# Optimization experiments

Measured on AMD Instinct MI355X. Metric: run time of the kernel, lower is better.

Reference implementation:

```python
import jax, jax.numpy as jnp
import numpy as np

AVG_STEP_WEIGHTING = 0.002


def _mean_rbf_kernel(a, b):
    """Mean over all (i,j) of exp(-||a_i - b_j||^2 / 2), features flattened.

    Equivalent to the original per-row loop: (1/N) * sum_i mean_j k(b, a_i).
    Uses the Gram trick to avoid materializing (N, M, D) intermediates.
    """
    A = a.reshape(a.shape[0], -1)  # (N, D)
    B = b.reshape(b.shape[0], -1)  # (M, D)
    sq_a = jnp.sum(A * A, axis=1)  # (N,)
    sq_b = jnp.sum(B * B, axis=1)  # (M,)
    # (N, M) pairwise squared distances; clamp tiny negatives from fp error
    d2 = jnp.maximum(sq_a[:, None] + sq_b[None, :] - 2.0 * (A @ B.T), 0.0)
    return jnp.mean(jnp.exp(-0.5 * d2))


def setup_inputs() -> dict:
    key = jax.random.key(0)
    kx, ky = jax.random.split(key)
    N, M, D1, D2 = 4096, 4096, 24, 8
    x = jax.random.normal(kx, (N, D1, D2), dtype=jnp.float32)
    y = jax.random.normal(ky, (M, D1, D2), dtype=jnp.float32)
    avg_step = jnp.asarray(5.0, dtype=jnp.float32)
    return {"x": x, "y": y, "avg_step": avg_step}


def reference(x, y, avg_step):
    XX = _mean_rbf_kernel(x, x)
    XY = _mean_rbf_kernel(x, y)
    YY = _mean_rbf_kernel(y, y)
    mmd = XX + YY - 2.0 * XY
    loss = mmd + (jnp.maximum(jnp.asarray(1.0, x.dtype), avg_step) - 1.0) * AVG_STEP_WEIGHTING
    return (loss, mmd)
```

## Files before the change

### kernel.cpp

```cpp
#include <hip/hip_runtime.h>
#include <hip/hip_bf16.h>

typedef __attribute__((ext_vector_type(8))) short short8;
typedef __attribute__((ext_vector_type(4))) float float4v;

#define N_ROWS 4096
#define K_DIM  192
#define TILE   128
#define NT     32
#define NSYM   528
#define NBLK   2080
#define LDSS   104
#define C1     (-0.72134752044448179f)
#define LOG2E  (1.4426950408889634f)

__global__ void prep_kernel(const float* __restrict__ x, const float* __restrict__ y,
                            __hip_bfloat16* __restrict__ xb, __hip_bfloat16* __restrict__ yb,
                            float* __restrict__ sqx, float* __restrict__ sqy)
{
    int w    = (blockIdx.x * blockDim.x + threadIdx.x) >> 6;
    int lane = threadIdx.x & 63;
    if (w >= 2 * N_ROWS) return;
    const float*      src = (w < N_ROWS) ? (x + (size_t)w * K_DIM) : (y + (size_t)(w - N_ROWS) * K_DIM);
    __hip_bfloat16*   dst = (w < N_ROWS) ? (xb + (size_t)w * K_DIM) : (yb + (size_t)(w - N_ROWS) * K_DIM);
    float s = 0.f;
    #pragma unroll
    for (int i = 0; i < 3; ++i) {
        float f = src[lane + 64 * i];
        __hip_bfloat16 h = __float2bfloat16(f);
        dst[lane + 64 * i] = h;
        float fb = __bfloat162float(h);
        s += fb * fb;
    }
    #pragma unroll
    for (int off = 32; off; off >>= 1) s += __shfl_down(s, off, 64);
    if (lane == 0) {
        if (w < N_ROWS) sqx[w] = s; else sqy[w - N_ROWS] = s;
    }
}

__global__ void gram_kernel(const __hip_bfloat16* __restrict__ xb, const __hip_bfloat16* __restrict__ yb,
                            const float* __restrict__ sqx, const float* __restrict__ sqy,
                            float* __restrict__ partials)
{
    __shared__ short lA[TILE * LDSS];
    __shared__ short lB[TILE * LDSS];
    __shared__ float wred[4];

    const short* xbs = (const short*)xb;
    const short* ybs = (const short*)yb;

    int id = blockIdx.x;
    const short *A, *B; const float *sa, *sb;
    int bi, bj;
    float weight = 1.0f;
    if (id < 2 * NSYM) {
        int t;
        if (id < NSYM) { t = id;        A = xbs; B = xbs; sa = sqx; sb = sqx; }
        else           { t = id - NSYM; A = ybs; B = ybs; sa = sqy; sb = sqy; }
        bi = 0;
        while (t >= NT - bi) { t -= NT - bi; ++bi; }
        bj = bi + t;
        if (bi != bj) weight = 2.0f;
    } else {
        int t = id - 2 * NSYM;
        bi = t >> 5; bj = t & 31;
        A = xbs; B = ybs; sa = sqx; sb = sqy;
    }
    const int abase = bi * TILE, bbase = bj * TILE;

    const int tid  = threadIdx.x;
    const int lane = tid & 63, w = tid >> 6;
    const int wm   = w >> 1,  wn = w & 1;
    const int m15  = lane & 15, quad = lane >> 4;

    float4v acc[4][4];
    #pragma unroll
    for (int i = 0; i < 4; ++i)
        #pragma unroll
        for (int j = 0; j < 4; ++j) acc[i][j] = (float4v){0.f, 0.f, 0.f, 0.f};

    for (int s = 0; s < 2; ++s) {
        const int k0 = s * 96;
        if (s) __syncthreads();
        #pragma unroll
        for (int it = 0; it < 6; ++it) {
            int c   = it * 256 + tid;
            int row = c / 12;
            int cw  = c - row * 12;
            uint4 va = *(const uint4*)(A + ((size_t)(abase + row) * K_DIM + k0 + cw * 8));
            uint4 vb = *(const uint4*)(B + ((size_t)(bbase + row) * K_DIM + k0 + cw * 8));
            *(uint4*)((char*)lA + row * (LDSS * 2) + cw * 16) = va;
            *(uint4*)((char*)lB + row * (LDSS * 2) + cw * 16) = vb;
        }
        __syncthreads();
        #pragma unroll
        for (int ks = 0; ks < 3; ++ks) {
            short8 af[4], bfr[4];
            const int colb = (ks * 32 + quad * 8) * 2;
            #pragma unroll
            for (int tm = 0; tm < 4; ++tm)
                af[tm] = *(const short8*)((const char*)lA + (wm * 64 + tm * 16 + m15) * (LDSS * 2) + colb);
            #pragma unroll
            for (int tn = 0; tn < 4; ++tn)
                bfr[tn] = *(const short8*)((const char*)lB + (wn * 64 + tn * 16 + m15) * (LDSS * 2) + colb);
            #pragma unroll
            for (int tm = 0; tm < 4; ++tm)
                #pragma unroll
                for (int tn = 0; tn < 4; ++tn)
                    acc[tm][tn] = __builtin_amdgcn_mfma_f32_16x16x32_bf16(af[tm], bfr[tn], acc[tm][tn], 0, 0, 0);
        }
    }

    float u[16], v[4];
    #pragma unroll
    for (int tm = 0; tm < 4; ++tm)
        #pragma unroll
        for (int r = 0; r < 4; ++r)
            u[tm * 4 + r] = C1 * sa[abase + wm * 64 + tm * 16 + quad * 4 + r];
    #pragma unroll
    for (int tn = 0; tn < 4; ++tn)
        v[tn] = C1 * sb[bbase + wn * 64 + tn * 16 + m15];

    float lsum = 0.f;
    #pragma unroll
    for (int tm = 0; tm < 4; ++tm)
        #pragma unroll
        for (int tn = 0; tn < 4; ++tn)
            #pragma unroll
            for (int r = 0; r < 4; ++r) {
                float g  = acc[tm][tn][r];
                float sv = fminf(u[tm * 4 + r] + v[tn] + LOG2E * g, 0.f);
                lsum += exp2f(sv);
            }

    #pragma unroll
    for (int off = 32; off; off >>= 1) lsum += __shfl_down(lsum, off, 64);
    if (lane == 0) wred[w] = lsum;
    __syncthreads();
    if (tid == 0) partials[id] = weight * (wred[0] + wred[1] + wred[2] + wred[3]);
}

__global__ void final_kernel(const float* __restrict__ partials, const float* __restrict__ avg_step,
                             float* __restrict__ out)
{
    __shared__ float red[3][4];
    int tid = threadIdx.x, lane = tid & 63, w = tid >> 6;
    float s0 = 0.f, s1 = 0.f, s2 = 0.f;
    for (int i = tid; i < NSYM; i += 256) s0 += partials[i];
    for (int i = tid; i < NSYM; i += 256) s1 += partials[NSYM + i];
    for (int i = tid; i < 1024; i += 256) s2 += partials[2 * NSYM + i];
    #pragma unroll
    for (int off = 32; off; off >>= 1) {
        s0 += __shfl_down(s0, off, 64);
        s1 += __shfl_down(s1, off, 64);
        s2 += __shfl_down(s2, off, 64);
    }
    if (lane == 0) { red[0][w] = s0; red[1][w] = s1; red[2][w] = s2; }
    __syncthreads();
    if (tid == 0) {
        float sxx = red[0][0] + red[0][1] + red[0][2] + red[0][3];
        float syy = red[1][0] + red[1][1] + red[1][2] + red[1][3];
        float sxy = red[2][0] + red[2][1] + red[2][2] + red[2][3];
        const float inv = 1.0f / 16777216.0f;
        float XX = sxx * inv, YY = syy * inv, XY = sxy * inv;
        float mmd  = XX + YY - 2.0f * XY;
        float stepv = fmaxf(1.0f, avg_step[0]);
        float loss = mmd + (stepv - 1.0f) * 0.002f;
        out[0] = loss;
        out[1] = mmd;
    }
}

extern "C" void kernel_launch(void* const* d_in, const int* in_sizes, int n_in,
                              void* d_out, int out_size, void* d_ws, size_t ws_size,
                              hipStream_t stream)
{
    const float* x        = (const float*)d_in[0];
    const float* y        = (const float*)d_in[1];
    const float* avg_step = (const float*)d_in[2];

    char* ws = (char*)d_ws;
    __hip_bfloat16* xb       = (__hip_bfloat16*)(ws);
    __hip_bfloat16* yb       = (__hip_bfloat16*)(ws + 1572864);
    float*          sqx      = (float*)(ws + 3145728);
    float*          sqy      = (float*)(ws + 3162112);
    float*          partials = (float*)(ws + 3178496);

    prep_kernel<<<2048, 256, 0, stream>>>(x, y, xb, yb, sqx, sqy);
    gram_kernel<<<NBLK, 256, 0, stream>>>(xb, yb, sqx, sqy, partials);
    final_kernel<<<1, 256, 0, stream>>>(partials, avg_step, (float*)d_out);
}
```

Baseline: 94.55 us.

## Use direct global-to-LDS loads, skip negligible exps, fuse final reduction

Tile loads now go straight from global memory into LDS through global_load_lds into a rotated, unpadded layout, and the second K-half load is issued after the first half's MFMAs. Whole 4-element groups whose log2 exponent is below -40 for every lane skip the exp2 work, using a wave ballot. This targets the large number of near-zero kernel values. The separate final kernel is removed: blocks add their partials into three global sums with atomics, and the last block, found through an atomic counter that the prep kernel resets, writes the outputs. A launch-bounds hint is also added. The trade-offs are float-atomic ordering nondeterminism and a tiny approximation from the dropped terms.

```diff
diff --git a/kernel.cpp b/kernel.cpp
--- a/kernel.cpp
+++ b/kernel.cpp
@@ -10,14 +10,26 @@
 #define NT     32
 #define NSYM   528
 #define NBLK   2080
-#define LDSS   104
 #define C1     (-0.72134752044448179f)
 #define LOG2E  (1.4426950408889634f)
 
+typedef const __attribute__((address_space(1))) unsigned int* gp_t;
+typedef __attribute__((address_space(3))) unsigned int* lp_t;
+
+__device__ __forceinline__ void gload16(const void* g, void* l) {
+    __builtin_amdgcn_global_load_lds((gp_t)g, (lp_t)l, 16, 0, 0);
+}
+
+__device__ __forceinline__ int div12(int x) {
+    return (x * 683) >> 13;
+}
+
 __global__ void prep_kernel(const float* __restrict__ x, const float* __restrict__ y,
                             __hip_bfloat16* __restrict__ xb, __hip_bfloat16* __restrict__ yb,
-                            float* __restrict__ sqx, float* __restrict__ sqy)
+                            float* __restrict__ sqx, float* __restrict__ sqy,
+                            unsigned* __restrict__ ctrl )
 {
+    if (blockIdx.x == 0 && threadIdx.x < 4) ctrl[threadIdx.x] = 0u;
     int w    = (blockIdx.x * blockDim.x + threadIdx.x) >> 6;
     int lane = threadIdx.x & 63;
     if (w >= 2 * N_ROWS) return;
@@ -39,12 +51,14 @@
     }
 }
 
-__global__ void gram_kernel(const __hip_bfloat16* __restrict__ xb, const __hip_bfloat16* __restrict__ yb,
-                            const float* __restrict__ sqx, const float* __restrict__ sqy,
-                            float* __restrict__ partials)
+__global__ __launch_bounds__(256, 3)
+void gram_kernel(const __hip_bfloat16* __restrict__ xb, const __hip_bfloat16* __restrict__ yb,
+                 const float* __restrict__ sqx, const float* __restrict__ sqy,
+                 float* __restrict__ sums, unsigned* __restrict__ counter,
+                 const float* __restrict__ avg_step, float* __restrict__ out)
 {
-    __shared__ short lA[TILE * LDSS];
-    __shared__ short lB[TILE * LDSS];
+    __shared__ short lA[TILE * 96];
+    __shared__ short lB[TILE * 96];
     __shared__ float wred[4];
 
     const short* xbs = (const short*)xb;
@@ -52,12 +66,12 @@
 
     int id = blockIdx.x;
     const short *A, *B; const float *sa, *sb;
-    int bi, bj;
+    int bi, bj, cls;
     float weight = 1.0f;
     if (id < 2 * NSYM) {
         int t;
-        if (id < NSYM) { t = id;        A = xbs; B = xbs; sa = sqx; sb = sqx; }
-        else           { t = id - NSYM; A = ybs; B = ybs; sa = sqy; sb = sqy; }
+        if (id < NSYM) { t = id;        A = xbs; B = xbs; sa = sqx; sb = sqx; cls = 0; }
+        else           { t = id - NSYM; A = ybs; B = ybs; sa = sqy; sb = sqy; cls = 1; }
         bi = 0;
         while (t >= NT - bi) { t -= NT - bi; ++bi; }
         bj = bi + t;
@@ -65,7 +79,7 @@
     } else {
         int t = id - 2 * NSYM;
         bi = t >> 5; bj = t & 31;
-        A = xbs; B = ybs; sa = sqx; sb = sqy;
+        A = xbs; B = ybs; sa = sqx; sb = sqy; cls = 2;
     }
     const int abase = bi * TILE, bbase = bj * TILE;
 
@@ -74,101 +88,123 @@
     const int wm   = w >> 1,  wn = w & 1;
     const int m15  = lane & 15, quad = lane >> 4;
 
+    int rowoff[6];
+    #pragma unroll
+    for (int it = 0; it < 6; ++it) {
+        int ci  = it * 256 + tid;
+        int row = div12(ci);
+        int j   = ci - row * 12;
+        int rot = row - div12(row) * 12;
+        int t   = j + rot; if (t >= 12) t -= 12;
+        rowoff[it] = row * K_DIM + t * 8;
+    }
+    const short* Apan = A + (size_t)abase * K_DIM;
+    const short* Bpan = B + (size_t)bbase * K_DIM;
+    char* lAb = (char*)lA;
+    char* lBb = (char*)lB;
+
+    #pragma unroll
+    for (int it = 0; it < 6; ++it) {
+        int ldso = (it * 256 + w * 64) * 16;
+        gload16(Apan + rowoff[it], lAb + ldso);
+        gload16(Bpan + rowoff[it], lBb + ldso);
+    }
+
+    int adA[3][4], adB[3][4];
+    #pragma unroll
+    for (int tm = 0; tm < 4; ++tm) {
+        int rA = wm * 64 + tm * 16 + m15;
+        int mA = rA - div12(rA) * 12; int nA = (mA == 0) ? 0 : (12 - mA);
+        int rB = wn * 64 + tm * 16 + m15;
+        int mB = rB - div12(rB) * 12; int nB = (mB == 0) ? 0 : (12 - mB);
+        #pragma unroll
+        for (int ks = 0; ks < 3; ++ks) {
+            int c  = ks * 4 + quad;
+            int ja = c + nA; if (ja >= 12) ja -= 12;
+            int jb = c + nB; if (jb >= 12) jb -= 12;
+            adA[ks][tm] = rA * 192 + ja * 16;
+            adB[ks][tm] = rB * 192 + jb * 16;
+        }
+    }
+
+    float4v ua[4]; float vb4[4];
+    #pragma unroll
+    for (int tm = 0; tm < 4; ++tm)
+        ua[tm] = (*(const float4v*)&sa[abase + wm * 64 + tm * 16 + quad * 4]) * C1;
+    #pragma unroll
+    for (int tn = 0; tn < 4; ++tn)
+        vb4[tn] = C1 * sb[bbase + wn * 64 + tn * 16 + m15];
+
     float4v acc[4][4];
     #pragma unroll
     for (int i = 0; i < 4; ++i)
         #pragma unroll
         for (int j = 0; j < 4; ++j) acc[i][j] = (float4v){0.f, 0.f, 0.f, 0.f};
 
+    #pragma unroll
     for (int s = 0; s < 2; ++s) {
-        const int k0 = s * 96;
-        if (s) __syncthreads();
-        #pragma unroll
-        for (int it = 0; it < 6; ++it) {
-            int c   = it * 256 + tid;
-            int row = c / 12;
-            int cw  = c - row * 12;
-            uint4 va = *(const uint4*)(A + ((size_t)(abase + row) * K_DIM + k0 + cw * 8));
-            uint4 vb = *(const uint4*)(B + ((size_t)(bbase + row) * K_DIM + k0 + cw * 8));
-            *(uint4*)((char*)lA + row * (LDSS * 2) + cw * 16) = va;
-            *(uint4*)((char*)lB + row * (LDSS * 2) + cw * 16) = vb;
-        }
         __syncthreads();
         #pragma unroll
         for (int ks = 0; ks < 3; ++ks) {
             short8 af[4], bfr[4];
-            const int colb = (ks * 32 + quad * 8) * 2;
-            #pragma unroll
-            for (int tm = 0; tm < 4; ++tm)
-                af[tm] = *(const short8*)((const char*)lA + (wm * 64 + tm * 16 + m15) * (LDSS * 2) + colb);
-            #pragma unroll
-            for (int tn = 0; tn < 4; ++tn)
-                bfr[tn] = *(const short8*)((const char*)lB + (wn * 64 + tn * 16 + m15) * (LDSS * 2) + colb);
+            #pragma unroll
+            for (int tm = 0; tm < 4; ++tm) af[tm]  = *(const short8*)(lAb + adA[ks][tm]);
+            #pragma unroll
+            for (int tn = 0; tn < 4; ++tn) bfr[tn] = *(const short8*)(lBb + adB[ks][tn]);
             #pragma unroll
             for (int tm = 0; tm < 4; ++tm)
                 #pragma unroll
                 for (int tn = 0; tn < 4; ++tn)
                     acc[tm][tn] = __builtin_amdgcn_mfma_f32_16x16x32_bf16(af[tm], bfr[tn], acc[tm][tn], 0, 0, 0);
         }
-    }
-
-    float u[16], v[4];
+        if (s == 0) {
+            __syncthreads();
+            #pragma unroll
+            for (int it = 0; it < 6; ++it) {
+                int ldso = (it * 256 + w * 64) * 16;
+                gload16(Apan + 96 + rowoff[it], lAb + ldso);
+                gload16(Bpan + 96 + rowoff[it], lBb + ldso);
+            }
+        }
+    }
+
+    float lsum = 0.f;
     #pragma unroll
     for (int tm = 0; tm < 4; ++tm)
         #pragma unroll
-        for (int r = 0; r < 4; ++r)
-            u[tm * 4 + r] = C1 * sa[abase + wm * 64 + tm * 16 + quad * 4 + r];
-    #pragma unroll
-    for (int tn = 0; tn < 4; ++tn)
-        v[tn] = C1 * sb[bbase + wn * 64 + tn * 16 + m15];
-
-    float lsum = 0.f;
-    #pragma unroll
-    for (int tm = 0; tm < 4; ++tm)
-        #pragma unroll
-        for (int tn = 0; tn < 4; ++tn)
-            #pragma unroll
-            for (int r = 0; r < 4; ++r) {
-                float g  = acc[tm][tn][r];
-                float sv = fminf(u[tm * 4 + r] + v[tn] + LOG2E * g, 0.f);
-                lsum += exp2f(sv);
+        for (int tn = 0; tn < 4; ++tn) {
+            float vv = vb4[tn];
+            float s0 = fminf(ua[tm][0] + vv + LOG2E * acc[tm][tn][0], 0.f);
+            float s1 = fminf(ua[tm][1] + vv + LOG2E * acc[tm][tn][1], 0.f);
+            float s2 = fminf(ua[tm][2] + vv + LOG2E * acc[tm][tn][2], 0.f);
+            float s3 = fminf(ua[tm][3] + vv + LOG2E * acc[tm][tn][3], 0.f);
+            float mx = fmaxf(fmaxf(s0, s1), fmaxf(s2, s3));
+            if (__ballot(mx > -40.f)) {
+                lsum += __builtin_amdgcn_exp2f(s0) + __builtin_amdgcn_exp2f(s1)
+                      + __builtin_amdgcn_exp2f(s2) + __builtin_amdgcn_exp2f(s3);
             }
+        }
 
     #pragma unroll
     for (int off = 32; off; off >>= 1) lsum += __shfl_down(lsum, off, 64);
     if (lane == 0) wred[w] = lsum;
     __syncthreads();
-    if (tid == 0) partials[id] = weight * (wred[0] + wred[1] + wred[2] + wred[3]);
-}
-
-__global__ void final_kernel(const float* __restrict__ partials, const float* __restrict__ avg_step,
-                             float* __restrict__ out)
-{
-    __shared__ float red[3][4];
-    int tid = threadIdx.x, lane = tid & 63, w = tid >> 6;
-    float s0 = 0.f, s1 = 0.f, s2 = 0.f;
-    for (int i = tid; i < NSYM; i += 256) s0 += partials[i];
-    for (int i = tid; i < NSYM; i += 256) s1 += partials[NSYM + i];
-    for (int i = tid; i < 1024; i += 256) s2 += partials[2 * NSYM + i];
-    #pragma unroll
-    for (int off = 32; off; off >>= 1) {
-        s0 += __shfl_down(s0, off, 64);
-        s1 += __shfl_down(s1, off, 64);
-        s2 += __shfl_down(s2, off, 64);
-    }
-    if (lane == 0) { red[0][w] = s0; red[1][w] = s1; red[2][w] = s2; }
-    __syncthreads();
     if (tid == 0) {
-        float sxx = red[0][0] + red[0][1] + red[0][2] + red[0][3];
-        float syy = red[1][0] + red[1][1] + red[1][2] + red[1][3];
-        float sxy = red[2][0] + red[2][1] + red[2][2] + red[2][3];
-        const float inv = 1.0f / 16777216.0f;
-        float XX = sxx * inv, YY = syy * inv, XY = sxy * inv;
-        float mmd  = XX + YY - 2.0f * XY;
-        float stepv = fmaxf(1.0f, avg_step[0]);
-        float loss = mmd + (stepv - 1.0f) * 0.002f;
-        out[0] = loss;
-        out[1] = mmd;
+        float p = weight * (wred[0] + wred[1] + wred[2] + wred[3]);
+        atomicAdd(&sums[cls], p);
+        __threadfence();
+        unsigned done = atomicAdd(counter, 1u);
+        if (done == NBLK - 1) {
+            __threadfence();
+            float sxx = atomicAdd(&sums[0], 0.0f);
+            float syy = atomicAdd(&sums[1], 0.0f);
+            float sxy = atomicAdd(&sums[2], 0.0f);
+            const float inv = 1.0f / 16777216.0f;
+            float mmd   = (sxx + syy - 2.0f * sxy) * inv;
+            float stepv = fmaxf(1.0f, avg_step[0]);
+            out[0] = mmd + (stepv - 1.0f) * 0.002f;
+            out[1] = mmd;
+        }
     }
 }
 
@@ -181,13 +217,14 @@
     const float* avg_step = (const float*)d_in[2];
 
     char* ws = (char*)d_ws;
-    __hip_bfloat16* xb       = (__hip_bfloat16*)(ws);
-    __hip_bfloat16* yb       = (__hip_bfloat16*)(ws + 1572864);
-    float*          sqx      = (float*)(ws + 3145728);
-    float*          sqy      = (float*)(ws + 3162112);
-    float*          partials = (float*)(ws + 3178496);
-
-    prep_kernel<<<2048, 256, 0, stream>>>(x, y, xb, yb, sqx, sqy);
-    gram_kernel<<<NBLK, 256, 0, stream>>>(xb, yb, sqx, sqy, partials);
-    final_kernel<<<1, 256, 0, stream>>>(partials, avg_step, (float*)d_out);
-}
+    __hip_bfloat16* xb      = (__hip_bfloat16*)(ws);
+    __hip_bfloat16* yb      = (__hip_bfloat16*)(ws + 1572864);
+    float*          sqx     = (float*)(ws + 3145728);
+    float*          sqy     = (float*)(ws + 3162112);
+    float*          sums    = (float*)(ws + 3178496);
+    unsigned*       counter = (unsigned*)(ws + 3178508);
+
+    prep_kernel<<<2048, 256, 0, stream>>>(x, y, xb, yb, sqx, sqy, (unsigned*)sums);
+    gram_kernel<<<NBLK, 256, 0, stream>>>(xb, yb, sqx, sqy, sums, counter,
+                                          avg_step, (float*)d_out);
+}
```

After: 129.4 us. 1.37x slower.

## Use 128x256 tiles with 512 threads, staged double buffer, and skip negligible exps

Applied to the files above, without the earlier changes.

Each block now computes a 128x256 output tile with 8 waves, halving the block count and reusing the A tile across two B tiles. The second K-half is loaded from global memory into registers while the first half's MFMAs run, and it goes to a separate LDS stage, so one barrier disappears. The exp epilogue skips a 4-element group when every lane's exponent is below -40, which removes most transcendental work for far-apart pairs. Symmetric tiles use per-wave weights (0, 1 or 2) to handle the diagonal and the padded edge. The cost is larger LDS use (about 160 KB dynamic) and wave-divergent branching in the epilogue.

```diff
diff --git a/kernel.cpp b/kernel.cpp
--- a/kernel.cpp
+++ b/kernel.cpp
@@ -6,11 +6,12 @@
 
 #define N_ROWS 4096
 #define K_DIM  192
-#define TILE   128
 #define NT     32
-#define NSYM   528
-#define NBLK   2080
-#define LDSS   104
+#define NXX    272
+#define NBLK   1056
+#define STRE   104
+#define STAGE_BYTES (384 * STRE * 2)
+#define LDS_TOTAL   (2 * STAGE_BYTES + 32)
 #define C1     (-0.72134752044448179f)
 #define LOG2E  (1.4426950408889634f)
 
@@ -39,106 +40,157 @@
     }
 }
 
-__global__ void gram_kernel(const __hip_bfloat16* __restrict__ xb, const __hip_bfloat16* __restrict__ yb,
-                            const float* __restrict__ sqx, const float* __restrict__ sqy,
-                            float* __restrict__ partials)
-{
-    __shared__ short lA[TILE * LDSS];
-    __shared__ short lB[TILE * LDSS];
-    __shared__ float wred[4];
-
+extern __shared__ char smem[];
+
+__global__ __launch_bounds__(512, 2)
+void gram_kernel(const __hip_bfloat16* __restrict__ xb, const __hip_bfloat16* __restrict__ yb,
+                 const float* __restrict__ sqx, const float* __restrict__ sqy,
+                 float* __restrict__ partials)
+{
     const short* xbs = (const short*)xb;
     const short* ybs = (const short*)yb;
 
     int id = blockIdx.x;
     const short *A, *B; const float *sa, *sb;
-    int bi, bj;
-    float weight = 1.0f;
-    if (id < 2 * NSYM) {
+    int bi, bj0, ntiles, sym;
+    if (id < 2 * NXX) {
         int t;
-        if (id < NSYM) { t = id;        A = xbs; B = xbs; sa = sqx; sb = sqx; }
-        else           { t = id - NSYM; A = ybs; B = ybs; sa = sqy; sb = sqy; }
+        if (id < NXX) { t = id;       A = xbs; B = xbs; sa = sqx; sb = sqx; }
+        else          { t = id - NXX; A = ybs; B = ybs; sa = sqy; sb = sqy; }
         bi = 0;
-        while (t >= NT - bi) { t -= NT - bi; ++bi; }
-        bj = bi + t;
-        if (bi != bj) weight = 2.0f;
+        for (;;) { int nb = (33 - bi) >> 1; if (t < nb) break; t -= nb; ++bi; }
+        bj0 = bi + 2 * t;
+        ntiles = (bj0 + 1 < NT) ? 2 : 1;
+        sym = 1;
     } else {
-        int t = id - 2 * NSYM;
-        bi = t >> 5; bj = t & 31;
-        A = xbs; B = ybs; sa = sqx; sb = sqy;
-    }
-    const int abase = bi * TILE, bbase = bj * TILE;
+        int t = id - 2 * NXX;
+        bi = t >> 4; bj0 = (t & 15) * 2; ntiles = 2;
+        A = xbs; B = ybs; sa = sqx; sb = sqy; sym = 0;
+    }
+    const int abase = bi * 128, bbase = bj0 * 128;
 
     const int tid  = threadIdx.x;
     const int lane = tid & 63, w = tid >> 6;
-    const int wm   = w >> 1,  wn = w & 1;
+    const int wm   = w >> 2,  wn = w & 3;
     const int m15  = lane & 15, quad = lane >> 4;
 
+    const short* gsrc[9];
+    int ldst[9];
+    #pragma unroll
+    for (int i = 0; i < 9; ++i) {
+        int c   = tid + 512 * i;
+        int row = (c * 10923) >> 17;
+        int cw  = c - row * 12;
+        const short* P; int gr;
+        if (row < 128) { P = A; gr = abase + row; }
+        else           { P = B; gr = bbase + row - 128; if (gr > N_ROWS - 1) gr = N_ROWS - 1; }
+        gsrc[i] = P + (size_t)gr * K_DIM + cw * 8;
+        ldst[i] = row * (STRE * 2) + cw * 16;
+    }
+
+    uint4 v0[9];
+    #pragma unroll
+    for (int i = 0; i < 9; ++i) v0[i] = *(const uint4*)(gsrc[i]);
+
+    float4v ua[4]; float vb4[4];
+    #pragma unroll
+    for (int tm = 0; tm < 4; ++tm)
+        ua[tm] = (*(const float4v*)&sa[abase + wm * 64 + tm * 16 + quad * 4]) * C1;
+    #pragma unroll
+    for (int tn = 0; tn < 4; ++tn) {
+        int ci = bbase + wn * 64 + tn * 16 + m15;
+        if (ci > N_ROWS - 1) ci = N_ROWS - 1;
+        vb4[tn] = C1 * sb[ci];
+    }
+
+    float weight = 1.0f;
+    if (sym) {
+        int sub = wn >> 1;
+        weight = (sub >= ntiles) ? 0.0f : (((bj0 + sub) == bi) ? 1.0f : 2.0f);
+    }
+
+    #pragma unroll
+    for (int i = 0; i < 9; ++i) *(uint4*)(smem + ldst[i]) = v0[i];
+    __syncthreads();
+
+    uint4 v1[9];
+    #pragma unroll
+    for (int i = 0; i < 9; ++i) v1[i] = *(const uint4*)(gsrc[i] + 96);
+
+    int offA[4], offB[4];
+    #pragma unroll
+    for (int tm = 0; tm < 4; ++tm)
+        offA[tm] = (wm * 64 + tm * 16 + m15) * (STRE * 2) + quad * 16;
+    #pragma unroll
+    for (int tn = 0; tn < 4; ++tn)
+        offB[tn] = (128 + wn * 64 + tn * 16 + m15) * (STRE * 2) + quad * 16;
+
     float4v acc[4][4];
     #pragma unroll
     for (int i = 0; i < 4; ++i)
         #pragma unroll
         for (int j = 0; j < 4; ++j) acc[i][j] = (float4v){0.f, 0.f, 0.f, 0.f};
 
-    for (int s = 0; s < 2; ++s) {
-        const int k0 = s * 96;
-        if (s) __syncthreads();
-        #pragma unroll
-        for (int it = 0; it < 6; ++it) {
-            int c   = it * 256 + tid;
-            int row = c / 12;
-            int cw  = c - row * 12;
-            uint4 va = *(const uint4*)(A + ((size_t)(abase + row) * K_DIM + k0 + cw * 8));
-            uint4 vb = *(const uint4*)(B + ((size_t)(bbase + row) * K_DIM + k0 + cw * 8));
-            *(uint4*)((char*)lA + row * (LDSS * 2) + cw * 16) = va;
-            *(uint4*)((char*)lB + row * (LDSS * 2) + cw * 16) = vb;
-        }
-        __syncthreads();
-        #pragma unroll
-        for (int ks = 0; ks < 3; ++ks) {
-            short8 af[4], bfr[4];
-            const int colb = (ks * 32 + quad * 8) * 2;
-            #pragma unroll
-            for (int tm = 0; tm < 4; ++tm)
-                af[tm] = *(const short8*)((const char*)lA + (wm * 64 + tm * 16 + m15) * (LDSS * 2) + colb);
+    #pragma unroll
+    for (int ks = 0; ks < 3; ++ks) {
+        short8 af[4], bfr[4];
+        #pragma unroll
+        for (int tm = 0; tm < 4; ++tm) af[tm]  = *(const short8*)(smem + offA[tm] + ks * 64);
+        #pragma unroll
+        for (int tn = 0; tn < 4; ++tn) bfr[tn] = *(const short8*)(smem + offB[tn] + ks * 64);
+        #pragma unroll
+        for (int tm = 0; tm < 4; ++tm)
             #pragma unroll
             for (int tn = 0; tn < 4; ++tn)
-                bfr[tn] = *(const short8*)((const char*)lB + (wn * 64 + tn * 16 + m15) * (LDSS * 2) + colb);
+                acc[tm][tn] = __builtin_amdgcn_mfma_f32_16x16x32_bf16(af[tm], bfr[tn], acc[tm][tn], 0, 0, 0);
+    }
+
+    #pragma unroll
+    for (int i = 0; i < 9; ++i) *(uint4*)(smem + STAGE_BYTES + ldst[i]) = v1[i];
+    __syncthreads();
+
+    #pragma unroll
+    for (int ks = 0; ks < 3; ++ks) {
+        short8 af[4], bfr[4];
+        #pragma unroll
+        for (int tm = 0; tm < 4; ++tm) af[tm]  = *(const short8*)(smem + STAGE_BYTES + offA[tm] + ks * 64);
+        #pragma unroll
+        for (int tn = 0; tn < 4; ++tn) bfr[tn] = *(const short8*)(smem + STAGE_BYTES + offB[tn] + ks * 64);
+        #pragma unroll
+        for (int tm = 0; tm < 4; ++tm)
             #pragma unroll
-            for (int tm = 0; tm < 4; ++tm)
-                #pragma unroll
-                for (int tn = 0; tn < 4; ++tn)
-                    acc[tm][tn] = __builtin_amdgcn_mfma_f32_16x16x32_bf16(af[tm], bfr[tn], acc[tm][tn], 0, 0, 0);
+            for (int tn = 0; tn < 4; ++tn)
+                acc[tm][tn] = __builtin_amdgcn_mfma_f32_16x16x32_bf16(af[tm], bfr[tn], acc[tm][tn], 0, 0, 0);
+    }
+
+    float lsum = 0.f;
+    #pragma unroll
+    for (int tm = 0; tm < 4; ++tm)
+        #pragma unroll
+        for (int tn = 0; tn < 4; ++tn) {
+            float vv = vb4[tn];
+            float s0 = fminf(ua[tm][0] + vv + LOG2E * acc[tm][tn][0], 0.f);
+            float s1 = fminf(ua[tm][1] + vv + LOG2E * acc[tm][tn][1], 0.f);
+            float s2 = fminf(ua[tm][2] + vv + LOG2E * acc[tm][tn][2], 0.f);
+            float s3 = fminf(ua[tm][3] + vv + LOG2E * acc[tm][tn][3], 0.f);
+            float mx = fmaxf(fmaxf(s0, s1), fmaxf(s2, s3));
+            if (__ballot(mx > -40.f)) {
+                lsum += __builtin_amdgcn_exp2f(s0) + __builtin_amdgcn_exp2f(s1)
+                      + __builtin_amdgcn_exp2f(s2) + __builtin_amdgcn_exp2f(s3);
+            }
         }
-    }
-
-    float u[16], v[4];
-    #pragma unroll
-    for (int tm = 0; tm < 4; ++tm)
-        #pragma unroll
-        for (int r = 0; r < 4; ++r)
-            u[tm * 4 + r] = C1 * sa[abase + wm * 64 + tm * 16 + quad * 4 + r];
-    #pragma unroll
-    for (int tn = 0; tn < 4; ++tn)
-        v[tn] = C1 * sb[bbase + wn * 64 + tn * 16 + m15];
-
-    float lsum = 0.f;
-    #pragma unroll
-    for (int tm = 0; tm < 4; ++tm)
-        #pragma unroll
-        for (int tn = 0; tn < 4; ++tn)
-            #pragma unroll
-            for (int r = 0; r < 4; ++r) {
-                float g  = acc[tm][tn][r];
-                float sv = fminf(u[tm * 4 + r] + v[tn] + LOG2E * g, 0.f);
-                lsum += exp2f(sv);
-            }
 
     #pragma unroll
     for (int off = 32; off; off >>= 1) lsum += __shfl_down(lsum, off, 64);
-    if (lane == 0) wred[w] = lsum;
-    __syncthreads();
-    if (tid == 0) partials[id] = weight * (wred[0] + wred[1] + wred[2] + wred[3]);
+    float* wred = (float*)(smem + 2 * STAGE_BYTES);
+    if (lane == 0) wred[w] = weight * lsum;
+    __syncthreads();
+    if (tid == 0) {
+        float p = 0.f;
+        #pragma unroll
+        for (int i = 0; i < 8; ++i) p += wred[i];
+        partials[id] = p;
+    }
 }
 
 __global__ void final_kernel(const float* __restrict__ partials, const float* __restrict__ avg_step,
@@ -147,9 +199,9 @@
     __shared__ float red[3][4];
     int tid = threadIdx.x, lane = tid & 63, w = tid >> 6;
     float s0 = 0.f, s1 = 0.f, s2 = 0.f;
-    for (int i = tid; i < NSYM; i += 256) s0 += partials[i];
-    for (int i = tid; i < NSYM; i += 256) s1 += partials[NSYM + i];
-    for (int i = tid; i < 1024; i += 256) s2 += partials[2 * NSYM + i];
+    for (int i = tid; i < NXX; i += 256) s0 += partials[i];
+    for (int i = tid; i < NXX; i += 256) s1 += partials[NXX + i];
+    for (int i = tid; i < 512; i += 256) s2 += partials[2 * NXX + i];
     #pragma unroll
     for (int off = 32; off; off >>= 1) {
         s0 += __shfl_down(s0, off, 64);
@@ -163,11 +215,9 @@
         float syy = red[1][0] + red[1][1] + red[1][2] + red[1][3];
         float sxy = red[2][0] + red[2][1] + red[2][2] + red[2][3];
         const float inv = 1.0f / 16777216.0f;
-        float XX = sxx * inv, YY = syy * inv, XY = sxy * inv;
-        float mmd  = XX + YY - 2.0f * XY;
+        float mmd   = (sxx + syy - 2.0f * sxy) * inv;
         float stepv = fmaxf(1.0f, avg_step[0]);
-        float loss = mmd + (stepv - 1.0f) * 0.002f;
-        out[0] = loss;
+        out[0] = mmd + (stepv - 1.0f) * 0.002f;
         out[1] = mmd;
     }
 }
@@ -187,7 +237,10 @@
     float*          sqy      = (float*)(ws + 3162112);
     float*          partials = (float*)(ws + 3178496);
 
+    hipFuncSetAttribute(reinterpret_cast<const void*>(gram_kernel),
+                        hipFuncAttributeMaxDynamicSharedMemorySize, LDS_TOTAL);
+
     prep_kernel<<<2048, 256, 0, stream>>>(x, y, xb, yb, sqx, sqy);
-    gram_kernel<<<NBLK, 256, 0, stream>>>(xb, yb, sqx, sqy, partials);
+    gram_kernel<<<NBLK, 512, LDS_TOTAL, stream>>>(xb, yb, sqx, sqy, partials);
     final_kernel<<<1, 256, 0, stream>>>(partials, avg_step, (float*)d_out);
 }
```

Measured after the change: 96.33 us. About the same (+1.9%).

## Use direct global-to-LDS loads with swizzled layout and prefetch second K half

Applied to the files above, without the earlier changes.

Replaces the register-staged global-to-LDS copies with global_load_lds direct transfers into a swizzled, unpadded LDS layout. The second K half is issued into a separate LDS region before computing on the first, so its load overlaps the first half's MFMAs. The epilogue vectorizes the norm loads, uses the raw hardware exp2, and skips the exponentials for 4-element groups whose arguments are all below -40 across the wave. LDS use roughly doubles to about 96KB per block, which may reduce how many blocks fit per CU.

```diff
diff --git a/kernel.cpp b/kernel.cpp
--- a/kernel.cpp
+++ b/kernel.cpp
@@ -6,13 +6,22 @@
 
 #define N_ROWS 4096
 #define K_DIM  192
-#define TILE   128
 #define NT     32
 #define NSYM   528
 #define NBLK   2080
-#define LDSS   104
+#define REG_A0 0
+#define REG_B0 24576
+#define REG_S1 49152
+#define LDS_TOTAL (98304 + 32)
 #define C1     (-0.72134752044448179f)
 #define LOG2E  (1.4426950408889634f)
+
+typedef const __attribute__((address_space(1))) unsigned int* gp_t;
+typedef __attribute__((address_space(3))) unsigned int* lp_t;
+
+__device__ __forceinline__ void gload16(const void* g, char* l) {
+    __builtin_amdgcn_global_load_lds((gp_t)g, (lp_t)l, 16, 0, 0);
+}
 
 __global__ void prep_kernel(const float* __restrict__ x, const float* __restrict__ y,
                             __hip_bfloat16* __restrict__ xb, __hip_bfloat16* __restrict__ yb,
@@ -39,14 +48,13 @@
     }
 }
 
-__global__ void gram_kernel(const __hip_bfloat16* __restrict__ xb, const __hip_bfloat16* __restrict__ yb,
-                            const float* __restrict__ sqx, const float* __restrict__ sqy,
-                            float* __restrict__ partials)
-{
-    __shared__ short lA[TILE * LDSS];
-    __shared__ short lB[TILE * LDSS];
-    __shared__ float wred[4];
-
+extern __shared__ char smem[];
+
+__global__ __launch_bounds__(256)
+void gram_kernel(const __hip_bfloat16* __restrict__ xb, const __hip_bfloat16* __restrict__ yb,
+                 const float* __restrict__ sqx, const float* __restrict__ sqy,
+                 float* __restrict__ partials)
+{
     const short* xbs = (const short*)xb;
     const short* ybs = (const short*)yb;
 
@@ -67,78 +75,124 @@
         bi = t >> 5; bj = t & 31;
         A = xbs; B = ybs; sa = sqx; sb = sqy;
     }
-    const int abase = bi * TILE, bbase = bj * TILE;
+    const int abase = bi * 128, bbase = bj * 128;
 
     const int tid  = threadIdx.x;
     const int lane = tid & 63, w = tid >> 6;
     const int wm   = w >> 1,  wn = w & 1;
     const int m15  = lane & 15, quad = lane >> 4;
 
+    int offG[6];
+    #pragma unroll
+    for (int i = 0; i < 6; ++i) {
+        int c  = i * 256 + tid;
+        int r  = (c * 683) >> 13;
+        int jp = c - 12 * r;
+        int js = (jp < 8) ? (jp ^ (r & 7)) : (8 + ((jp + ((r >> 1) & 3)) & 3));
+        offG[i] = r * 384 + js * 16;
+    }
+    const char* ApanB = (const char*)(A + (size_t)abase * K_DIM);
+    const char* BpanB = (const char*)(B + (size_t)bbase * K_DIM);
+
+    #pragma unroll
+    for (int i = 0; i < 6; ++i) {
+        int d = (i * 256 + w * 64) * 16;
+        gload16(ApanB + offG[i],       smem + REG_A0 + d);
+        gload16(BpanB + offG[i],       smem + REG_B0 + d);
+    }
+
+    int adA[3][4], adB[3][4];
+    #pragma unroll
+    for (int tm = 0; tm < 4; ++tm) {
+        int rA = wm * 64 + tm * 16 + m15;
+        int kA = rA & 7, mA = (rA >> 1) & 3, rbA = rA * 192;
+        int rB = wn * 64 + tm * 16 + m15;
+        int kB = rB & 7, mB = (rB >> 1) & 3, rbB = rB * 192;
+        adA[0][tm] = rbA + ((quad)      ^ kA) * 16;
+        adA[1][tm] = rbA + ((4 + quad)  ^ kA) * 16;
+        adA[2][tm] = rbA + (8 + ((quad + 4 - mA) & 3)) * 16;
+        adB[0][tm] = rbB + ((quad)      ^ kB) * 16;
+        adB[1][tm] = rbB + ((4 + quad)  ^ kB) * 16;
+        adB[2][tm] = rbB + (8 + ((quad + 4 - mB) & 3)) * 16;
+    }
+
+    float4v ua[4]; float vb4[4];
+    #pragma unroll
+    for (int tm = 0; tm < 4; ++tm)
+        ua[tm] = (*(const float4v*)&sa[abase + wm * 64 + tm * 16 + quad * 4]) * C1;
+    #pragma unroll
+    for (int tn = 0; tn < 4; ++tn)
+        vb4[tn] = C1 * sb[bbase + wn * 64 + tn * 16 + m15];
+
     float4v acc[4][4];
     #pragma unroll
     for (int i = 0; i < 4; ++i)
         #pragma unroll
         for (int j = 0; j < 4; ++j) acc[i][j] = (float4v){0.f, 0.f, 0.f, 0.f};
 
-    for (int s = 0; s < 2; ++s) {
-        const int k0 = s * 96;
-        if (s) __syncthreads();
-        #pragma unroll
-        for (int it = 0; it < 6; ++it) {
-            int c   = it * 256 + tid;
-            int row = c / 12;
-            int cw  = c - row * 12;
-            uint4 va = *(const uint4*)(A + ((size_t)(abase + row) * K_DIM + k0 + cw * 8));
-            uint4 vb = *(const uint4*)(B + ((size_t)(bbase + row) * K_DIM + k0 + cw * 8));
-            *(uint4*)((char*)lA + row * (LDSS * 2) + cw * 16) = va;
-            *(uint4*)((char*)lB + row * (LDSS * 2) + cw * 16) = vb;
-        }
-        __syncthreads();
-        #pragma unroll
-        for (int ks = 0; ks < 3; ++ks) {
-            short8 af[4], bfr[4];
-            const int colb = (ks * 32 + quad * 8) * 2;
-            #pragma unroll
-            for (int tm = 0; tm < 4; ++tm)
-                af[tm] = *(const short8*)((const char*)lA + (wm * 64 + tm * 16 + m15) * (LDSS * 2) + colb);
+    __syncthreads();
+
+    #pragma unroll
+    for (int i = 0; i < 6; ++i) {
+        int d = (i * 256 + w * 64) * 16;
+        gload16(ApanB + offG[i] + 192, smem + REG_S1 + d);
+        gload16(BpanB + offG[i] + 192, smem + REG_S1 + 24576 + d);
+    }
+
+    #pragma unroll
+    for (int t = 0; t < 3; ++t) {
+        short8 af[4], bfr[4];
+        #pragma unroll
+        for (int tm = 0; tm < 4; ++tm) af[tm]  = *(const short8*)(smem + REG_A0 + adA[t][tm]);
+        #pragma unroll
+        for (int tn = 0; tn < 4; ++tn) bfr[tn] = *(const short8*)(smem + REG_B0 + adB[t][tn]);
+        #pragma unroll
+        for (int tm = 0; tm < 4; ++tm)
             #pragma unroll
             for (int tn = 0; tn < 4; ++tn)
-                bfr[tn] = *(const short8*)((const char*)lB + (wn * 64 + tn * 16 + m15) * (LDSS * 2) + colb);
+                acc[tm][tn] = __builtin_amdgcn_mfma_f32_16x16x32_bf16(af[tm], bfr[tn], acc[tm][tn], 0, 0, 0);
+    }
+
+    __syncthreads();
+
+    #pragma unroll
+    for (int t = 0; t < 3; ++t) {
+        short8 af[4], bfr[4];
+        #pragma unroll
+        for (int tm = 0; tm < 4; ++tm) af[tm]  = *(const short8*)(smem + REG_S1 + adA[t][tm]);
+        #pragma unroll
+        for (int tn = 0; tn < 4; ++tn) bfr[tn] = *(const short8*)(smem + REG_S1 + 24576 + adB[t][tn]);
+        #pragma unroll
+        for (int tm = 0; tm < 4; ++tm)
             #pragma unroll
-            for (int tm = 0; tm < 4; ++tm)
-                #pragma unroll
-                for (int tn = 0; tn < 4; ++tn)
-                    acc[tm][tn] = __builtin_amdgcn_mfma_f32_16x16x32_bf16(af[tm], bfr[tn], acc[tm][tn], 0, 0, 0);
+            for (int tn = 0; tn < 4; ++tn)
+                acc[tm][tn] = __builtin_amdgcn_mfma_f32_16x16x32_bf16(af[tm], bfr[tn], acc[tm][tn], 0, 0, 0);
+    }
+
+    float lsum = 0.f;
+    #pragma unroll
+    for (int tm = 0; tm < 4; ++tm)
+        #pragma unroll
+        for (int tn = 0; tn < 4; ++tn) {
+            float vv = vb4[tn];
+            float s0 = fminf(ua[tm][0] + vv + LOG2E * acc[tm][tn][0], 0.f);
+            float s1 = fminf(ua[tm][1] + vv + LOG2E * acc[tm][tn][1], 0.f);
+            float s2 = fminf(ua[tm][2] + vv + LOG2E * acc[tm][tn][2], 0.f);
+            float s3 = fminf(ua[tm][3] + vv + LOG2E * acc[tm][tn][3], 0.f);
+            float mx = fmaxf(fmaxf(s0, s1), fmaxf(s2, s3));
+            if (__ballot(mx > -40.f)) {
+                lsum += __builtin_amdgcn_exp2f(s0) + __builtin_amdgcn_exp2f(s1)
+                      + __builtin_amdgcn_exp2f(s2) + __builtin_amdgcn_exp2f(s3);
+            }
         }
-    }
-
-    float u[16], v[4];
-    #pragma unroll
-    for (int tm = 0; tm < 4; ++tm)
-        #pragma unroll
-        for (int r = 0; r < 4; ++r)
-            u[tm * 4 + r] = C1 * sa[abase + wm * 64 + tm * 16 + quad * 4 + r];
-    #pragma unroll
-    for (int tn = 0; tn < 4; ++tn)
-        v[tn] = C1 * sb[bbase + wn * 64 + tn * 16 + m15];
-
-    float lsum = 0.f;
-    #pragma unroll
-    for (int tm = 0; tm < 4; ++tm)
-        #pragma unroll
-        for (int tn = 0; tn < 4; ++tn)
-            #pragma unroll
-            for (int r = 0; r < 4; ++r) {
-                float g  = acc[tm][tn][r];
-                float sv = fminf(u[tm * 4 + r] + v[tn] + LOG2E * g, 0.f);
-                lsum += exp2f(sv);
-            }
 
     #pragma unroll
     for (int off = 32; off; off >>= 1) lsum += __shfl_down(lsum, off, 64);
+    float* wred = (float*)(smem + 98304);
     if (lane == 0) wred[w] = lsum;
     __syncthreads();
-    if (tid == 0) partials[id] = weight * (wred[0] + wred[1] + wred[2] + wred[3]);
+    if (tid == 0)
+        partials[id] = weight * (wred[0] + wred[1] + wred[2] + wred[3]);
 }
 
 __global__ void final_kernel(const float* __restrict__ partials, const float* __restrict__ avg_step,
@@ -163,11 +217,9 @@
         float syy = red[1][0] + red[1][1] + red[1][2] + red[1][3];
         float sxy = red[2][0] + red[2][1] + red[2][2] + red[2][3];
         const float inv = 1.0f / 16777216.0f;
-        float XX = sxx * inv, YY = syy * inv, XY = sxy * inv;
-        float mmd  = XX + YY - 2.0f * XY;
+        float mmd   = (sxx + syy - 2.0f * sxy) * inv;
         float stepv = fmaxf(1.0f, avg_step[0]);
-        float loss = mmd + (stepv - 1.0f) * 0.002f;
-        out[0] = loss;
+        out[0] = mmd + (stepv - 1.0f) * 0.002f;
         out[1] = mmd;
     }
 }
@@ -187,7 +239,10 @@
     float*          sqy      = (float*)(ws + 3162112);
     float*          partials = (float*)(ws + 3178496);
 
+    hipFuncSetAttribute(reinterpret_cast<const void*>(gram_kernel),
+                        hipFuncAttributeMaxDynamicSharedMemorySize, LDS_TOTAL);
+
     prep_kernel<<<2048, 256, 0, stream>>>(x, y, xb, yb, sqx, sqy);
-    gram_kernel<<<NBLK, 256, 0, stream>>>(xb, yb, sqx, sqy, partials);
+    gram_kernel<<<NBLK, 256, LDS_TOTAL, stream>>>(xb, yb, sqx, sqy, partials);
     final_kernel<<<1, 256, 0, stream>>>(partials, avg_step, (float*)d_out);
 }
```

Measured after the change: 102.9 us. +8.8%, slower.
